# Kernel tuning notes

Measured on AMD Instinct MI355X. Metric: run time of the kernel, lower is better.

The kernel has to match this reference:

```python
import jax, jax.numpy as jnp
import numpy as np

D_MODEL = 1024
H = 16
D_HEAD = D_MODEL // H  # 64
RANK = 32
ALPHA = 1.0


def _lora_linear(x, W, b, dW, dB):
    # merged weight: W + alpha * (dB @ dW), then x @ W_merged.T + b
    Wm = W + ALPHA * (dB @ dW)
    return x @ Wm.T + b


def setup_inputs() -> dict:
    key = jax.random.key(0)
    ks = jax.random.split(key, 20)
    inp = {"x": jax.random.normal(ks[0], (2, 2048, D_MODEL), dtype=jnp.float32)}
    i = 1
    for name in ("q", "k", "v", "o"):
        inp[f"{name}_W"] = jax.random.normal(ks[i], (D_MODEL, D_MODEL), dtype=jnp.float32) * 0.02; i += 1
        inp[f"{name}_b"] = jnp.zeros((D_MODEL,), dtype=jnp.float32)
        inp[f"{name}_dW"] = jax.random.normal(ks[i], (RANK, D_MODEL), dtype=jnp.float32) * 0.01; i += 1
        inp[f"{name}_dB"] = jax.random.normal(ks[i], (D_MODEL, RANK), dtype=jnp.float32) * 0.01; i += 1
    return inp


def reference(x, q_W, q_b, q_dW, q_dB, k_W, k_b, k_dW, k_dB,
              v_W, v_b, v_dW, v_dB, o_W, o_b, o_dW, o_dB):
    b_s, n, _ = x.shape
    # LoRA-merged QKV projections
    q = _lora_linear(x, q_W, q_b, q_dW, q_dB).reshape(b_s, n, H, D_HEAD)
    k = _lora_linear(x, k_W, k_b, k_dW, k_dB).reshape(b_s, n, H, D_HEAD)
    v = _lora_linear(x, v_W, v_b, v_dW, v_dB).reshape(b_s, n, H, D_HEAD)
    scale = 1.0 / np.sqrt(D_HEAD).astype(np.float32)
    # att: [b, h, nq, nk]
    att = jnp.einsum('bqhd,bkhd->bhqk', q, k) * scale
    att = jax.nn.softmax(att, axis=-1)  # dropout = identity (eval mode)
    out = jnp.einsum('bhqk,bkhd->bqhd', att, v).reshape(b_s, n, H * D_HEAD)
    return _lora_linear(out, o_W, o_b, o_dW, o_dB)
```

## Files before the change

kernel.cpp:

```cpp
#include <hip/hip_runtime.h>

typedef unsigned short ushort_t;
typedef unsigned int u32;
typedef __attribute__((ext_vector_type(8))) short short8;
typedef __attribute__((ext_vector_type(4))) float floatx4;
typedef __attribute__((ext_vector_type(16))) float floatx16;
typedef __attribute__((ext_vector_type(2))) unsigned int uintx2;
typedef __attribute__((ext_vector_type(4))) unsigned int uintx4;

typedef const __attribute__((address_space(1))) u32* gptr_t;
typedef __attribute__((address_space(3))) u32* lptr_t;

__device__ __forceinline__ void async_copy16(void* lds, const void* g) {
  __builtin_amdgcn_global_load_lds((gptr_t)g, (lptr_t)lds, 16, 0, 0);
}

__device__ __forceinline__ ushort_t f2bf(float f) {
  u32 u = __float_as_uint(f);
  u += 0x7fffu + ((u >> 16) & 1u);
  return (ushort_t)(u >> 16);
}

__device__ __forceinline__ floatx4 mfma16(short8 a, short8 b, floatx4 c) {
  return __builtin_amdgcn_mfma_f32_16x16x32_bf16(a, b, c, 0, 0, 0);
}

__device__ __forceinline__ floatx16 mfma32(short8 a, short8 b, floatx16 c) {
  return __builtin_amdgcn_mfma_f32_32x32x16_bf16(a, b, c, 0, 0, 0);
}

__device__ __forceinline__ u32 cvt_pk_bf16(float lo, float hi) {
  u32 r;
  asm("v_cvt_pk_bf16_f32 %0, %1, %2" : "=v"(r) : "v"(lo), "v"(hi));
  return r;
}

__device__ __forceinline__ short8 mkfrag(u32 x0, u32 x1, u32 x2, u32 x3) {
  uintx2 ra = __builtin_amdgcn_permlane32_swap(x0, x2, false, false);
  uintx2 rb = __builtin_amdgcn_permlane32_swap(x1, x3, false, false);
  union { uintx4 u; short8 s; } t;
  t.u[0] = ra[0]; t.u[1] = rb[0]; t.u[2] = ra[1]; t.u[3] = rb[1];
  return t.s;
}

struct alignas(16) F4 { float a, b, c, d; };
struct alignas(8) U4 { ushort_t a, b, c, d; };

#define QSCALE 0.18033688011112043f

__global__ __launch_bounds__(256) void prep_kernel(
    const float* __restrict__ x, ushort_t* __restrict__ xs,
    const float* __restrict__ W0, const float* __restrict__ dW0, const float* __restrict__ dB0,
    const float* __restrict__ W1, const float* __restrict__ dW1, const float* __restrict__ dB1,
    const float* __restrict__ W2, const float* __restrict__ dW2, const float* __restrict__ dB2,
    const float* __restrict__ W3, const float* __restrict__ dW3, const float* __restrict__ dB3,
    ushort_t* __restrict__ Wm) {
  const int bid = blockIdx.x;
  if (bid < 4096) {
    int i = bid * 256 + threadIdx.x;
    F4 v = ((const F4*)x)[i];
    U4 hh = {f2bf(v.a), f2bf(v.b), f2bf(v.c), f2bf(v.d)};
    ((U4*)xs)[i] = hh;
    return;
  }
  const int t = bid - 4096;
  const int layer = t >> 7, sub = t & 127;
  const float* W = (layer == 0) ? W0 : (layer == 1) ? W1 : (layer == 2) ? W2 : W3;
  const float* dW = (layer == 0) ? dW0 : (layer == 1) ? dW1 : (layer == 2) ? dW2 : dW3;
  const float* dB = (layer == 0) ? dB0 : (layer == 1) ? dB1 : (layer == 2) ? dB2 : dB3;
  ushort_t* Wh = Wm + (size_t)layer * 1024 * 1024;
  const int ot = sub * 8;
  const int d0 = threadIdx.x * 4;
  float acc[8][4] = {};
  for (int r = 0; r < 32; ++r) {
    F4 w = *(const F4*)&dW[r * 1024 + d0];
    float wv[4] = {w.a, w.b, w.c, w.d};
#pragma unroll
    for (int o = 0; o < 8; ++o) {
      float s = dB[(ot + o) * 32 + r];
#pragma unroll
      for (int j = 0; j < 4; ++j) acc[o][j] += s * wv[j];
    }
  }
#pragma unroll
  for (int o = 0; o < 8; ++o) {
    F4 w = *(const F4*)&W[(ot + o) * 1024 + d0];
    U4 hh = {f2bf(w.a + acc[o][0]), f2bf(w.b + acc[o][1]),
             f2bf(w.c + acc[o][2]), f2bf(w.d + acc[o][3])};
    *(U4*)&Wh[(ot + o) * 1024 + d0] = hh;
  }
}

template <int MODE, int TN>
__global__ __launch_bounds__(256) void gemm_bt(
    const ushort_t* __restrict__ A, const ushort_t* __restrict__ B,
    const float* __restrict__ b0, const float* __restrict__ b1,
    const float* __restrict__ b2,
    ushort_t* __restrict__ C, ushort_t* __restrict__ vth,
    float* __restrict__ Cf, const int M, const int N, const int K) {
  constexpr int NT2 = TN / 32;
  __shared__ __align__(16) ushort_t lA[2][128 * 32], lB[2][TN * 32];
  const int tid = threadIdx.x;
  const int wave = tid >> 6, lane = tid & 63;
  const int lo4 = lane & 15, quad = lane >> 4;
  const int n0 = blockIdx.x * TN, m0 = blockIdx.y * 128;
  const int wm = (wave >> 1) * 64, wn = (wave & 1) * (TN / 2);

  floatx4 acc[4][NT2];
  const floatx4 zero4 = {0.f, 0.f, 0.f, 0.f};
#pragma unroll
  for (int mt = 0; mt < 4; ++mt)
#pragma unroll
    for (int nt = 0; nt < NT2; ++nt) acc[mt][nt] = zero4;

  const int strow = lane >> 2;
  const int stcol = (lane & 3) * 8;

  const int NTILES = K >> 5;
  {
#pragma unroll
    for (int i = 0; i < 2; ++i) {
      const int g = wave * 2 + i;
      async_copy16(&lA[0][g * 512], A + (size_t)(m0 + g * 16 + strow) * K + stcol);
    }
#pragma unroll
    for (int i = 0; i < TN / 64; ++i) {
      const int g = wave * (TN / 64) + i;
      async_copy16(&lB[0][g * 512], B + (size_t)(n0 + g * 16 + strow) * K + stcol);
    }
  }
  __syncthreads();

  for (int t = 0; t < NTILES; ++t) {
    const int cur = t & 1;
    if (t + 1 < NTILES) {
      const int kk = (t + 1) << 5;
#pragma unroll
      for (int i = 0; i < 2; ++i) {
        const int g = wave * 2 + i;
        async_copy16(&lA[cur ^ 1][g * 512], A + (size_t)(m0 + g * 16 + strow) * K + kk + stcol);
      }
#pragma unroll
      for (int i = 0; i < TN / 64; ++i) {
        const int g = wave * (TN / 64) + i;
        async_copy16(&lB[cur ^ 1][g * 512], B + (size_t)(n0 + g * 16 + strow) * K + kk + stcol);
      }
    }
    short8 a_[4], b_[NT2];
#pragma unroll
    for (int t2 = 0; t2 < 4; ++t2)
      a_[t2] = *(const short8*)&lA[cur][(wm + t2 * 16 + lo4) * 32 + quad * 8];
#pragma unroll
    for (int t2 = 0; t2 < NT2; ++t2)
      b_[t2] = *(const short8*)&lB[cur][(wn + t2 * 16 + lo4) * 32 + quad * 8];
#pragma unroll
    for (int mt = 0; mt < 4; ++mt)
#pragma unroll
      for (int nt = 0; nt < NT2; ++nt) acc[mt][nt] = mfma16(a_[mt], b_[nt], acc[mt][nt]);
    if (t + 1 < NTILES) __syncthreads();
  }

#pragma unroll
  for (int nt = 0; nt < NT2; ++nt) {
    const int col = n0 + wn + nt * 16 + lo4;
    float bias;
    if (MODE == 0)
      bias = (col < 1024) ? b0[col] : (col < 2048) ? b1[col - 1024] : b2[col - 2048];
    else
      bias = b0[col];
#pragma unroll
    for (int mt = 0; mt < 4; ++mt)
#pragma unroll
      for (int r = 0; r < 4; ++r) {
        const int row = m0 + wm + mt * 16 + quad * 4 + r;
        float c = acc[mt][nt][r] + bias;
        if (MODE == 0) {
          if (col < 1024) c *= QSCALE;
          ushort_t hv = f2bf(c);
          if (col < 2048) {
            C[(size_t)row * 2048 + col] = hv;
          } else {
            const int d = col - 2048;
            const size_t vrow = (size_t)(((row >> 11) * 16 + (d >> 6)) * 64 + (d & 63));
            vth[vrow * 2048 + (row & 2047)] = hv;
          }
        } else {
          Cf[(size_t)row * N + col] = c;
        }
      }
  }
}

__global__ __launch_bounds__(512, 4) void attn_kernel(
    const ushort_t* __restrict__ qk, const ushort_t* __restrict__ vt,
    ushort_t* __restrict__ at) {
  __shared__ __align__(16) ushort_t Kh[2][2][64 * 64];
  __shared__ __align__(16) ushort_t Vh[2][2][64 * 64];
  const int bid = blockIdx.x;
  const int xcd = bid & 7, g = bid >> 3;
  const int bh = xcd * 4 + (g >> 4), qt = g & 15;
  const int b = bh >> 4, h = bh & 15;
  const int tid = threadIdx.x;
  const int wave = tid >> 6, lane = tid & 63;
  const int rowg = wave & 3, half = wave >> 2;
  const int l31 = lane & 31, hi = lane >> 5, l7 = lane & 7;
  const int hi8 = hi * 8;

  short8 qf[4];
  {
    const ushort_t* gq =
        qk + (size_t)(b * 2048 + qt * 128 + rowg * 32 + l31) * 2048 + h * 64 + hi8;
#pragma unroll
    for (int st = 0; st < 4; ++st) qf[st] = *(const short8*)(gq + st * 16);
  }

  floatx16 O[2];
#pragma unroll
  for (int i = 0; i < 16; ++i) { O[0][i] = 0.f; O[1][i] = 0.f; }
  float l_acc[4] = {0.f, 0.f, 0.f, 0.f};

  const int stile = wave >> 1, spart = wave & 1;
  const int strow = lane >> 3;
  const int stswz = (l7 ^ strow) * 8;
  const ushort_t* Ksrc = qk + (size_t)b * 2048 * 2048 + 1024 + h * 64;
  const ushort_t* Vsrc = vt + (size_t)bh * 64 * 2048;

#define STAGE(buf, t_)                                                             \
  {                                                                                \
    const int kt_ = 2 * (t_) + (stile & 1);                                        \
    if (stile < 2) {                                                               \
      const ushort_t* s_ =                                                         \
          Ksrc + (size_t)(kt_ * 64 + spart * 32 + strow) * 2048 + stswz;           \
      ushort_t* d_ = &Kh[buf][stile & 1][spart * 32 * 64];                         \
      _Pragma("unroll") for (int i_ = 0; i_ < 4; ++i_)                             \
          async_copy16(d_ + i_ * 512, s_ + (size_t)i_ * 8 * 2048);                 \
    } else {                                                                       \
      const ushort_t* s_ =                                                         \
          Vsrc + (size_t)(spart * 32 + strow) * 2048 + kt_ * 64 + stswz;           \
      ushort_t* d_ = &Vh[buf][stile & 1][spart * 32 * 64];                         \
      _Pragma("unroll") for (int i_ = 0; i_ < 4; ++i_)                             \
          async_copy16(d_ + i_ * 512, s_ + (size_t)i_ * 8 * 2048);                 \
    }                                                                              \
  }

  STAGE(0, 0);
  __syncthreads();

  for (int t = 0; t < 16; ++t) {
    const int cur = t & 1;
    if (t + 1 < 16) STAGE(cur ^ 1, t + 1);

    floatx16 s0, s1;
#pragma unroll
    for (int i = 0; i < 16; ++i) { s0[i] = 0.f; s1[i] = 0.f; }
    __builtin_amdgcn_s_setprio(1);
#pragma unroll
    for (int st = 0; st < 4; ++st) {
      const int c = ((st * 2 + hi) ^ l7) * 8;
      s0 = mfma32(*(const short8*)&Kh[cur][half][l31 * 64 + c], qf[st], s0);
      s1 = mfma32(*(const short8*)&Kh[cur][half][(32 + l31) * 64 + c], qf[st], s1);
    }
    __builtin_amdgcn_s_setprio(0);

    u32 a0[8], a1[8];
#pragma unroll
    for (int j = 0; j < 8; ++j) {
      float p0a = __builtin_amdgcn_exp2f(s0[2 * j]);
      float p0b = __builtin_amdgcn_exp2f(s0[2 * j + 1]);
      float p1a = __builtin_amdgcn_exp2f(s1[2 * j]);
      float p1b = __builtin_amdgcn_exp2f(s1[2 * j + 1]);
      l_acc[j & 3] += (p0a + p0b) + (p1a + p1b);
      a0[j] = cvt_pk_bf16(p0a, p0b);
      a1[j] = cvt_pk_bf16(p1a, p1b);
    }

    short8 pb00 = mkfrag(a0[0], a0[1], a0[2], a0[3]);
    short8 pb01 = mkfrag(a0[4], a0[5], a0[6], a0[7]);
    short8 pb10 = mkfrag(a1[0], a1[1], a1[2], a1[3]);
    short8 pb11 = mkfrag(a1[4], a1[5], a1[6], a1[7]);

    __builtin_amdgcn_s_setprio(1);
#pragma unroll
    for (int dblk = 0; dblk < 2; ++dblk) {
      const int vr = (dblk * 32 + l31) * 64;
      O[dblk] = mfma32(*(const short8*)&Vh[cur][half][vr + ((0 + hi) ^ l7) * 8], pb00, O[dblk]);
      O[dblk] = mfma32(*(const short8*)&Vh[cur][half][vr + ((2 + hi) ^ l7) * 8], pb01, O[dblk]);
      O[dblk] = mfma32(*(const short8*)&Vh[cur][half][vr + ((4 + hi) ^ l7) * 8], pb10, O[dblk]);
      O[dblk] = mfma32(*(const short8*)&Vh[cur][half][vr + ((6 + hi) ^ l7) * 8], pb11, O[dblk]);
    }
    __builtin_amdgcn_s_setprio(0);
    if (t + 1 < 16) __syncthreads();
  }
#undef STAGE

  float l = (l_acc[0] + l_acc[1]) + (l_acc[2] + l_acc[3]);
  l += __shfl_xor(l, 32);

  float* Pf0 = (float*)&Kh[0][0][0];
  float* Pf1 = (float*)&Vh[0][0][0];
  __syncthreads();
  if (half == 1) {
    const int base = rowg * 1280 + lane * 20;
#pragma unroll
    for (int j = 0; j < 16; ++j) Pf0[base + j] = O[0][j];
#pragma unroll
    for (int j = 0; j < 16; ++j) Pf1[base + j] = O[1][j];
    Pf0[base + 16] = l;
  }
  __syncthreads();
  if (half == 0) {
    const int base = rowg * 1280 + lane * 20;
#pragma unroll
    for (int j = 0; j < 16; ++j) O[0][j] += Pf0[base + j];
#pragma unroll
    for (int j = 0; j < 16; ++j) O[1][j] += Pf1[base + j];
    l += Pf0[base + 16];
    const float linv = 1.f / l;
    ushort_t* out =
        at + (size_t)(b * 2048 + qt * 128 + rowg * 32 + l31) * 1024 + h * 64;
#pragma unroll
    for (int dblk = 0; dblk < 2; ++dblk)
#pragma unroll
      for (int gr = 0; gr < 4; ++gr) {
        U4 hh = {f2bf(O[dblk][4 * gr + 0] * linv), f2bf(O[dblk][4 * gr + 1] * linv),
                 f2bf(O[dblk][4 * gr + 2] * linv), f2bf(O[dblk][4 * gr + 3] * linv)};
        *(U4*)&out[dblk * 32 + gr * 8 + hi * 4] = hh;
      }
  }
}

extern "C" void kernel_launch(void* const* d_in, const int* in_sizes, int n_in,
                              void* d_out, int out_size, void* d_ws, size_t ws_size,
                              hipStream_t stream) {
  const float* x = (const float*)d_in[0];
  const float* qW = (const float*)d_in[1];
  const float* qb = (const float*)d_in[2];
  const float* qdW = (const float*)d_in[3];
  const float* qdB = (const float*)d_in[4];
  const float* kW = (const float*)d_in[5];
  const float* kb = (const float*)d_in[6];
  const float* kdW = (const float*)d_in[7];
  const float* kdB = (const float*)d_in[8];
  const float* vW = (const float*)d_in[9];
  const float* vb = (const float*)d_in[10];
  const float* vdW = (const float*)d_in[11];
  const float* vdB = (const float*)d_in[12];
  const float* oW = (const float*)d_in[13];
  const float* ob = (const float*)d_in[14];
  const float* odW = (const float*)d_in[15];
  const float* odB = (const float*)d_in[16];

  char* ws = (char*)d_ws;
  const size_t MB = 1024u * 1024u;
  const size_t WELEM = 1024u * 1024u;
  ushort_t* xs = (ushort_t*)(ws + 0 * MB);
  ushort_t* Wm = (ushort_t*)(ws + 8 * MB);
  ushort_t* qk = (ushort_t*)(ws + 16 * MB);
  ushort_t* vt = (ushort_t*)(ws + 32 * MB);
  ushort_t* at = xs;

  prep_kernel<<<4608, 256, 0, stream>>>(x, xs, qW, qdW, qdB, kW, kdW, kdB,
                                        vW, vdW, vdB, oW, odW, odB, Wm);
  gemm_bt<0, 128><<<dim3(24, 32), 256, 0, stream>>>(xs, Wm, qb, kb, vb,
                                                    qk, vt, nullptr, 4096, 3072, 1024);
  attn_kernel<<<512, 512, 0, stream>>>(qk, vt, at);
  gemm_bt<1, 64><<<dim3(16, 32), 256, 0, stream>>>(at, Wm + 3 * WELEM, ob, nullptr,
                                                   nullptr, nullptr, nullptr,
                                                   (float*)d_out, 4096, 1024, 1024);
}
```

Baseline: 220.3 us.

## Add dedicated 256x256-tile QKV GEMM with four-stage async LDS ring

```diff
diff --git a/kernel.cpp b/kernel.cpp
--- a/kernel.cpp
+++ b/kernel.cpp
@@ -88,6 +88,104 @@
     U4 hh = {f2bf(w.a + acc[o][0]), f2bf(w.b + acc[o][1]),
              f2bf(w.c + acc[o][2]), f2bf(w.d + acc[o][3])};
     *(U4*)&Wh[(ot + o) * 1024 + d0] = hh;
+  }
+}
+
+__global__ __launch_bounds__(512, 2) void gemm_qkv(
+    const ushort_t* __restrict__ A, const ushort_t* __restrict__ B,
+    const float* __restrict__ b0, const float* __restrict__ b1,
+    const float* __restrict__ b2, ushort_t* __restrict__ C,
+    ushort_t* __restrict__ vth) {
+  __shared__ __align__(16) ushort_t lA[4][256 * 32], lB[4][256 * 32];
+  const int tid = threadIdx.x;
+  const int wave = tid >> 6, lane = tid & 63;
+  const int lo4 = lane & 15, quad = lane >> 4;
+  const int n0 = blockIdx.x * 256, m0 = blockIdx.y * 256;
+  const int wm = (wave >> 2) * 128, wn = (wave & 3) * 64;
+  const int srow = lane >> 2;
+  const int sch = ((lane & 3) ^ ((lane >> 3) & 3)) * 8;
+  const int rdsw = (quad ^ ((lo4 >> 1) & 3)) * 8;
+
+  floatx4 acc[8][4];
+  const floatx4 zero4 = {0.f, 0.f, 0.f, 0.f};
+#pragma unroll
+  for (int mt = 0; mt < 8; ++mt)
+#pragma unroll
+    for (int nt = 0; nt < 4; ++nt) acc[mt][nt] = zero4;
+
+#define RING_STAGE(t_)                                                           \
+  {                                                                              \
+    const int kk_ = (t_) * 32;                                                   \
+    _Pragma("unroll") for (int i_ = 0; i_ < 2; ++i_) {                           \
+      const int rg_ = wave * 2 + i_;                                             \
+      async_copy16(&lA[(t_) & 3][rg_ * 512],                                     \
+                   A + (size_t)(m0 + rg_ * 16 + srow) * 1024 + kk_ + sch);       \
+      async_copy16(&lB[(t_) & 3][rg_ * 512],                                     \
+                   B + (size_t)(n0 + rg_ * 16 + srow) * 1024 + kk_ + sch);       \
+    }                                                                            \
+  }
+
+#define RING_COMPUTE(t_)                                                         \
+  {                                                                              \
+    const ushort_t* bufA_ = lA[(t_) & 3];                                        \
+    const ushort_t* bufB_ = lB[(t_) & 3];                                        \
+    short8 a_[8], b_[4];                                                         \
+    _Pragma("unroll") for (int mt_ = 0; mt_ < 8; ++mt_)                          \
+        a_[mt_] = *(const short8*)&bufA_[(wm + mt_ * 16 + lo4) * 32 + rdsw];     \
+    _Pragma("unroll") for (int nt_ = 0; nt_ < 4; ++nt_)                          \
+        b_[nt_] = *(const short8*)&bufB_[(wn + nt_ * 16 + lo4) * 32 + rdsw];     \
+    __builtin_amdgcn_s_setprio(1);                                               \
+    _Pragma("unroll") for (int mt_ = 0; mt_ < 8; ++mt_)                          \
+        _Pragma("unroll") for (int nt_ = 0; nt_ < 4; ++nt_)                      \
+            acc[mt_][nt_] = mfma16(a_[mt_], b_[nt_], acc[mt_][nt_]);             \
+    __builtin_amdgcn_s_setprio(0);                                               \
+  }
+
+#define RING_SYNC(vm_)                                       \
+  asm volatile("s_waitcnt vmcnt(" #vm_ ")" ::: "memory");    \
+  __builtin_amdgcn_s_barrier();                              \
+  __builtin_amdgcn_sched_barrier(0);
+
+  RING_STAGE(0);
+  RING_STAGE(1);
+  RING_STAGE(2);
+  RING_SYNC(8);
+
+  for (int t = 0; t < 29; ++t) {
+    RING_STAGE(t + 3);
+    RING_COMPUTE(t);
+    RING_SYNC(8);
+  }
+  RING_COMPUTE(29);
+  RING_SYNC(4);
+  RING_COMPUTE(30);
+  RING_SYNC(0);
+  RING_COMPUTE(31);
+#undef RING_STAGE
+#undef RING_COMPUTE
+#undef RING_SYNC
+
+#pragma unroll
+  for (int nt = 0; nt < 4; ++nt) {
+    const int col = n0 + wn + nt * 16 + lo4;
+    const float bias =
+        (col < 1024) ? b0[col] : (col < 2048) ? b1[col - 1024] : b2[col - 2048];
+#pragma unroll
+    for (int mt = 0; mt < 8; ++mt)
+#pragma unroll
+      for (int r = 0; r < 4; ++r) {
+        const int row = m0 + wm + mt * 16 + quad * 4 + r;
+        float c = acc[mt][nt][r] + bias;
+        if (col < 1024) c *= QSCALE;
+        ushort_t hv = f2bf(c);
+        if (col < 2048) {
+          C[(size_t)row * 2048 + col] = hv;
+        } else {
+          const int d = col - 2048;
+          const size_t vrow = (size_t)(((row >> 11) * 16 + (d >> 6)) * 64 + (d & 63));
+          vth[vrow * 2048 + (row & 2047)] = hv;
+        }
+      }
   }
 }
 
@@ -361,8 +459,7 @@
 
   prep_kernel<<<4608, 256, 0, stream>>>(x, xs, qW, qdW, qdB, kW, kdW, kdB,
                                         vW, vdW, vdB, oW, odW, odB, Wm);
-  gemm_bt<0, 128><<<dim3(24, 32), 256, 0, stream>>>(xs, Wm, qb, kb, vb,
-                                                    qk, vt, nullptr, 4096, 3072, 1024);
+  gemm_qkv<<<dim3(12, 16), 512, 0, stream>>>(xs, Wm, qb, kb, vb, qk, vt);
   attn_kernel<<<512, 512, 0, stream>>>(qk, vt, at);
   gemm_bt<1, 64><<<dim3(16, 32), 256, 0, stream>>>(at, Wm + 3 * WELEM, ob, nullptr,
                                                    nullptr, nullptr, nullptr,
```

Result: slower. 243.9 us (+10.7%).

## Compute softmax row sums via MFMA with ones and vectorize GEMM epilogue stores

Applied to the files above, without the earlier changes.

```diff
diff --git a/kernel.cpp b/kernel.cpp
--- a/kernel.cpp
+++ b/kernel.cpp
@@ -156,38 +156,53 @@
 #pragma unroll
     for (int mt = 0; mt < 4; ++mt)
 #pragma unroll
-      for (int nt = 0; nt < NT2; ++nt) acc[mt][nt] = mfma16(a_[mt], b_[nt], acc[mt][nt]);
+      for (int nt = 0; nt < NT2; ++nt)
+        acc[mt][nt] = (MODE == 0) ? mfma16(a_[mt], b_[nt], acc[mt][nt])
+                                  : mfma16(b_[nt], a_[mt], acc[mt][nt]);
     if (t + 1 < NTILES) __syncthreads();
   }
 
-#pragma unroll
-  for (int nt = 0; nt < NT2; ++nt) {
-    const int col = n0 + wn + nt * 16 + lo4;
-    float bias;
-    if (MODE == 0)
-      bias = (col < 1024) ? b0[col] : (col < 2048) ? b1[col - 1024] : b2[col - 2048];
-    else
-      bias = b0[col];
-#pragma unroll
-    for (int mt = 0; mt < 4; ++mt)
-#pragma unroll
-      for (int r = 0; r < 4; ++r) {
-        const int row = m0 + wm + mt * 16 + quad * 4 + r;
-        float c = acc[mt][nt][r] + bias;
-        if (MODE == 0) {
-          if (col < 1024) c *= QSCALE;
-          ushort_t hv = f2bf(c);
-          if (col < 2048) {
-            C[(size_t)row * 2048 + col] = hv;
-          } else {
-            const int d = col - 2048;
-            const size_t vrow = (size_t)(((row >> 11) * 16 + (d >> 6)) * 64 + (d & 63));
-            vth[vrow * 2048 + (row & 2047)] = hv;
+  if (MODE == 0) {
+#pragma unroll
+    for (int nt = 0; nt < NT2; ++nt) {
+      const int col = n0 + wn + nt * 16 + lo4;
+      const float bias =
+          (col < 1024) ? b0[col] : (col < 2048) ? b1[col - 1024] : b2[col - 2048];
+      if (col < 2048) {
+#pragma unroll
+        for (int mt = 0; mt < 4; ++mt)
+#pragma unroll
+          for (int r = 0; r < 4; ++r) {
+            const int row = m0 + wm + mt * 16 + quad * 4 + r;
+            float c = acc[mt][nt][r] + bias;
+            if (col < 1024) c *= QSCALE;
+            C[(size_t)row * 2048 + col] = f2bf(c);
           }
-        } else {
-          Cf[(size_t)row * N + col] = c;
+      } else {
+        const int d = col - 2048;
+#pragma unroll
+        for (int mt = 0; mt < 4; ++mt) {
+          const int rowb = m0 + wm + mt * 16 + quad * 4;
+          const size_t vrow = (size_t)(((rowb >> 11) * 16 + (d >> 6)) * 64 + (d & 63));
+          U4 hh = {f2bf(acc[mt][nt][0] + bias), f2bf(acc[mt][nt][1] + bias),
+                   f2bf(acc[mt][nt][2] + bias), f2bf(acc[mt][nt][3] + bias)};
+          *(U4*)&vth[vrow * 2048 + (rowb & 2047)] = hh;
         }
       }
+    }
+  } else {
+#pragma unroll
+    for (int nt = 0; nt < NT2; ++nt) {
+      const int col0 = n0 + wn + nt * 16 + quad * 4;
+      const F4 bv = *(const F4*)&b0[col0];
+#pragma unroll
+      for (int mt = 0; mt < 4; ++mt) {
+        const int row = m0 + wm + mt * 16 + lo4;
+        F4 o = {acc[mt][nt][0] + bv.a, acc[mt][nt][1] + bv.b,
+                acc[mt][nt][2] + bv.c, acc[mt][nt][3] + bv.d};
+        *(F4*)&Cf[(size_t)row * N + col0] = o;
+      }
+    }
   }
 }
 
@@ -214,10 +229,17 @@
     for (int st = 0; st < 4; ++st) qf[st] = *(const short8*)(gq + st * 16);
   }
 
-  floatx16 O[2];
-#pragma unroll
-  for (int i = 0; i < 16; ++i) { O[0][i] = 0.f; O[1][i] = 0.f; }
-  float l_acc[4] = {0.f, 0.f, 0.f, 0.f};
+  floatx16 O[2], Lacc;
+#pragma unroll
+  for (int i = 0; i < 16; ++i) { O[0][i] = 0.f; O[1][i] = 0.f; Lacc[i] = 0.f; }
+
+  short8 onesf;
+  {
+    union { uintx4 u; short8 s; } ou;
+    ou.u[0] = 0x3F803F80u; ou.u[1] = 0x3F803F80u;
+    ou.u[2] = 0x3F803F80u; ou.u[3] = 0x3F803F80u;
+    onesf = ou.s;
+  }
 
   const int stile = wave >> 1, spart = wave & 1;
   const int strow = lane >> 3;
@@ -265,13 +287,10 @@
     u32 a0[8], a1[8];
 #pragma unroll
     for (int j = 0; j < 8; ++j) {
-      float p0a = __builtin_amdgcn_exp2f(s0[2 * j]);
-      float p0b = __builtin_amdgcn_exp2f(s0[2 * j + 1]);
-      float p1a = __builtin_amdgcn_exp2f(s1[2 * j]);
-      float p1b = __builtin_amdgcn_exp2f(s1[2 * j + 1]);
-      l_acc[j & 3] += (p0a + p0b) + (p1a + p1b);
-      a0[j] = cvt_pk_bf16(p0a, p0b);
-      a1[j] = cvt_pk_bf16(p1a, p1b);
+      a0[j] = cvt_pk_bf16(__builtin_amdgcn_exp2f(s0[2 * j]),
+                          __builtin_amdgcn_exp2f(s0[2 * j + 1]));
+      a1[j] = cvt_pk_bf16(__builtin_amdgcn_exp2f(s1[2 * j]),
+                          __builtin_amdgcn_exp2f(s1[2 * j + 1]));
     }
 
     short8 pb00 = mkfrag(a0[0], a0[1], a0[2], a0[3]);
@@ -280,6 +299,10 @@
     short8 pb11 = mkfrag(a1[4], a1[5], a1[6], a1[7]);
 
     __builtin_amdgcn_s_setprio(1);
+    Lacc = mfma32(onesf, pb00, Lacc);
+    Lacc = mfma32(onesf, pb01, Lacc);
+    Lacc = mfma32(onesf, pb10, Lacc);
+    Lacc = mfma32(onesf, pb11, Lacc);
 #pragma unroll
     for (int dblk = 0; dblk < 2; ++dblk) {
       const int vr = (dblk * 32 + l31) * 64;
@@ -293,8 +316,7 @@
   }
 #undef STAGE
 
-  float l = (l_acc[0] + l_acc[1]) + (l_acc[2] + l_acc[3]);
-  l += __shfl_xor(l, 32);
+  float l = Lacc[0];
 
   float* Pf0 = (float*)&Kh[0][0][0];
   float* Pf1 = (float*)&Vh[0][0][0];
```

Measured after the change: 216.9 us. About the same (-1.6%).
